# Kernel tuning notes

Measured on AMD Instinct MI355X. Metric: run time of the kernel, lower is better.

The kernel has to match this reference:

```python
import jax, jax.numpy as jnp
import numpy as np

B, T, C, H = 8, 2048, 1024, 64  # batch, block_size(=seq), embedding_dim, head_size

def setup_inputs() -> dict:
    key = jax.random.key(0)
    kx, kk, kq, kv = jax.random.split(key, 4)
    s = 1.0 / np.sqrt(C)
    return {
        "x": jax.random.normal(kx, (B, T, C), dtype=jnp.float32),
        "Wk": jax.random.normal(kk, (C, H), dtype=jnp.float32) * s,
        "Wq": jax.random.normal(kq, (C, H), dtype=jnp.float32) * s,
        "Wv": jax.random.normal(kv, (C, H), dtype=jnp.float32) * s,
    }

def reference(x, Wk, Wq, Wv):
    # projections: [B,T,C] @ [C,H] -> [B,T,H]
    k = jnp.einsum("btc,ch->bth", x, Wk)
    q = jnp.einsum("btc,ch->bth", x, Wq)
    v = jnp.einsum("btc,ch->bth", x, Wv)
    # scores: [B,T,T], scaled by head_size^-0.5
    wei = jnp.einsum("bth,bsh->bts", q, k) * (k.shape[-1] ** -0.5)
    # causal mask (lower-triangular keep)
    causal = jnp.tril(jnp.ones((T, T), dtype=bool))
    wei = jnp.where(causal[None, :, :], wei, -jnp.inf)
    wei = jax.nn.softmax(wei, axis=-1)
    # dropout_rate=0.0 -> identity
    out = jnp.einsum("bts,bsh->bth", wei, v)
    return out
```

## Files before the change

### kernel.cpp

```cpp
#include <hip/hip_runtime.h>

#define NB 8
#define NT 2048
#define NC 1024
#define NH 64
#define BT (NB*NT)

typedef __bf16 bf16x8 __attribute__((ext_vector_type(8)));
typedef float  f32x4  __attribute__((ext_vector_type(4)));
typedef unsigned short us8 __attribute__((ext_vector_type(8)));

__device__ __forceinline__ unsigned short f2bf(float f) {
  unsigned u = __builtin_bit_cast(unsigned, f);
  u = (u + 0x7FFFu + ((u >> 16) & 1u)) >> 16;
  return (unsigned short)u;
}

__device__ __forceinline__ bf16x8 ld_frag(const unsigned short* p) {
  return __builtin_bit_cast(bf16x8, *(const us8*)p);
}

__global__ __launch_bounds__(256) void wconv_kernel(
    const float* __restrict__ Wk, const float* __restrict__ Wq,
    const float* __restrict__ Wv, unsigned short* __restrict__ Wt)
{
  __shared__ unsigned short T[64][72];
  const int t = threadIdx.x;
  const int mat = blockIdx.x >> 4;
  const int k0 = (blockIdx.x & 15) * 64;
  const float* __restrict__ W = (mat == 0) ? Wq : (mat == 1) ? Wk : Wv;
  const int kk = t >> 2, h0 = (t & 3) * 16;
  const float* src = &W[(size_t)(k0 + kk) * NH + h0];
#pragma unroll
  for (int j = 0; j < 4; ++j) {
    const float4 v = *(const float4*)(src + j*4);
    T[h0 + j*4 + 0][kk] = f2bf(v.x);
    T[h0 + j*4 + 1][kk] = f2bf(v.y);
    T[h0 + j*4 + 2][kk] = f2bf(v.z);
    T[h0 + j*4 + 3][kk] = f2bf(v.w);
  }
  __syncthreads();
  const int h = t >> 2, c0 = (t & 3) * 16;
  unsigned short* dst = &Wt[(size_t)(mat*64 + h) * NC + k0 + c0];
  *(us8*)dst       = *(const us8*)&T[h][c0];
  *(us8*)(dst + 8) = *(const us8*)&T[h][c0 + 8];
}

__global__ __launch_bounds__(512) void proj_kernel(
    const float* __restrict__ x, const unsigned short* __restrict__ Wt,
    unsigned short* __restrict__ qkv)
{
  __shared__ unsigned short Asm[64][72];
  __shared__ unsigned short Bsm[192][72];

  const int t = threadIdx.x, w = t >> 6, lane = t & 63;
  const int wm = w >> 1, wn = w & 1;
  const int m0 = blockIdx.x * 64;
  const int fr = lane & 15, fo = (lane >> 4) * 8;

  f32x4 acc[6];
#pragma unroll
  for (int n = 0; n < 6; ++n) acc[n] = (f32x4){0.f, 0.f, 0.f, 0.f};

  const int ar = t >> 3, akc = (t & 7) * 8;

  for (int k0 = 0; k0 < NC; k0 += 64) {
    {
      const float* src = &x[(size_t)(m0 + ar) * NC + k0 + akc];
      const float4 a = *(const float4*)src;
      const float4 b = *(const float4*)(src + 4);
      us8 u;
      u[0]=f2bf(a.x); u[1]=f2bf(a.y); u[2]=f2bf(a.z); u[3]=f2bf(a.w);
      u[4]=f2bf(b.x); u[5]=f2bf(b.y); u[6]=f2bf(b.z); u[7]=f2bf(b.w);
      *(us8*)&Asm[ar][akc] = u;
    }
#pragma unroll
    for (int i = 0; i < 3; ++i) {
      const int c = t + 512*i, r = c >> 3, kc = (c & 7) * 8;
      *(us8*)&Bsm[r][kc] = *(const us8*)&Wt[(size_t)r * NC + k0 + kc];
    }
    __syncthreads();

    bf16x8 af[2], bfr[2][6];
#pragma unroll
    for (int ks = 0; ks < 2; ++ks) {
      af[ks] = ld_frag(&Asm[wm*16 + fr][ks*32 + fo]);
#pragma unroll
      for (int n = 0; n < 6; ++n) bfr[ks][n] = ld_frag(&Bsm[wn*96 + n*16 + fr][ks*32 + fo]);
    }
#pragma unroll
    for (int ks = 0; ks < 2; ++ks)
#pragma unroll
      for (int n = 0; n < 6; ++n)
        acc[n] = __builtin_amdgcn_mfma_f32_16x16x32_bf16(af[ks], bfr[ks][n], acc[n], 0, 0, 0);
    __syncthreads();
  }

  const int rg = (lane >> 4) * 4;
  const int trow = m0 + wm*16 + rg;
#pragma unroll
  for (int n = 0; n < 6; ++n) {
    const int col = wn*96 + n*16;
    const int mat = col >> 6;
    const int h = (col & 63) + fr;
    if (mat < 2) {
      unsigned short* op = qkv + (size_t)mat * BT * NH;
#pragma unroll
      for (int r = 0; r < 4; ++r)
        op[(size_t)(trow + r) * NH + h] = f2bf(acc[n][r]);
    } else {
      unsigned short* vt = qkv + (size_t)2 * BT * NH;
#pragma unroll
      for (int r = 0; r < 4; ++r)
        vt[(size_t)h * BT + trow + r] = f2bf(acc[n][r]);
    }
  }
}

__global__ __launch_bounds__(256) void attn_kernel(
    const unsigned short* __restrict__ qkv, float* __restrict__ out)
{
  __shared__ unsigned short Psm[4][16][72];
  __shared__ float co[4][16][68];
  __shared__ float cl[4][16];

  const int t = threadIdx.x, w = t >> 6, lane = t & 63;
  const int b = blockIdx.y;
  const unsigned short* __restrict__ qp = qkv;
  const unsigned short* __restrict__ kp = qkv + (size_t)BT * NH;
  const unsigned short* __restrict__ vt = qkv + (size_t)2 * BT * NH;
  const int fr = lane & 15, fo = (lane >> 4) * 8, rg = (lane >> 4) * 4;

#pragma unroll 1
  for (int ph = 0; ph < 2; ++ph) {
    const int j = ph ? (127 - (int)blockIdx.x) : (int)blockIdx.x;
    const int q0 = j * 16;
    const int ntiles = (j >> 2) + 1;

    bf16x8 aq0, aq1;
    {
      const size_t qoff = ((size_t)b * NT + q0 + fr) * NH;
      aq0 = ld_frag(&qp[qoff + fo]);
      aq1 = ld_frag(&qp[qoff + 32 + fo]);
    }

    f32x4 o[4];
#pragma unroll
    for (int n = 0; n < 4; ++n) o[n] = (f32x4){0.f, 0.f, 0.f, 0.f};
    float lp[4] = {0.f, 0.f, 0.f, 0.f};

    for (int kt = w; kt < ntiles; kt += 4) {
      const int kv0 = kt * 64;

      f32x4 s[4];
#pragma unroll
      for (int n = 0; n < 4; ++n) s[n] = (f32x4){0.f, 0.f, 0.f, 0.f};
#pragma unroll
      for (int n = 0; n < 4; ++n) {
        const size_t koff = ((size_t)b*NT + kv0 + n*16 + fr) * NH + fo;
        s[n] = __builtin_amdgcn_mfma_f32_16x16x32_bf16(aq0, ld_frag(&kp[koff]), s[n], 0, 0, 0);
        s[n] = __builtin_amdgcn_mfma_f32_16x16x32_bf16(aq1, ld_frag(&kp[koff + 32]), s[n], 0, 0, 0);
      }

#pragma unroll
      for (int n = 0; n < 4; ++n)
#pragma unroll
        for (int r = 0; r < 4; ++r) s[n][r] = __expf(s[n][r] * 0.125f);

      if (kt == ntiles - 1) {
#pragma unroll
        for (int n = 0; n < 4; ++n) {
          const int col = kv0 + n*16 + fr;
#pragma unroll
          for (int r = 0; r < 4; ++r)
            if (col > q0 + rg + r) s[n][r] = 0.f;
        }
      }

#pragma unroll
      for (int r = 0; r < 4; ++r)
        lp[r] += (s[0][r] + s[1][r]) + (s[2][r] + s[3][r]);

#pragma unroll
      for (int n = 0; n < 4; ++n)
#pragma unroll
        for (int r = 0; r < 4; ++r)
          Psm[w][rg + r][n*16 + fr] = f2bf(s[n][r]);

      bf16x8 pa0 = ld_frag(&Psm[w][fr][fo]);
      bf16x8 pa1 = ld_frag(&Psm[w][fr][32 + fo]);

#pragma unroll
      for (int n = 0; n < 4; ++n) {
        const size_t voff = (size_t)(n*16 + fr) * BT + (size_t)b*NT + kv0 + fo;
        o[n] = __builtin_amdgcn_mfma_f32_16x16x32_bf16(pa0, ld_frag(&vt[voff]), o[n], 0, 0, 0);
        o[n] = __builtin_amdgcn_mfma_f32_16x16x32_bf16(pa1, ld_frag(&vt[voff + 32]), o[n], 0, 0, 0);
      }
    }

#pragma unroll
    for (int r = 0; r < 4; ++r) {
#pragma unroll
      for (int off = 1; off < 16; off <<= 1) lp[r] += __shfl_xor(lp[r], off);
    }
    if (fr == 0) {
#pragma unroll
      for (int r = 0; r < 4; ++r) cl[w][rg + r] = lp[r];
    }
#pragma unroll
    for (int n = 0; n < 4; ++n)
#pragma unroll
      for (int r = 0; r < 4; ++r) co[w][rg + r][n*16 + fr] = o[n][r];
    __syncthreads();

    {
      const int row = t >> 4, c0 = (t & 15) * 4;
      const float l = (cl[0][row] + cl[1][row]) + (cl[2][row] + cl[3][row]);
      const float inv = 1.f / l;
      float4 ov;
      ov.x = ((co[0][row][c0+0] + co[1][row][c0+0]) + (co[2][row][c0+0] + co[3][row][c0+0])) * inv;
      ov.y = ((co[0][row][c0+1] + co[1][row][c0+1]) + (co[2][row][c0+1] + co[3][row][c0+1])) * inv;
      ov.z = ((co[0][row][c0+2] + co[1][row][c0+2]) + (co[2][row][c0+2] + co[3][row][c0+2])) * inv;
      ov.w = ((co[0][row][c0+3] + co[1][row][c0+3]) + (co[2][row][c0+3] + co[3][row][c0+3])) * inv;
      *(float4*)&out[((size_t)b*NT + q0 + row) * NH + c0] = ov;
    }
    if (ph == 0) __syncthreads();
  }
}

extern "C" void kernel_launch(void* const* d_in, const int* in_sizes, int n_in,
                              void* d_out, int out_size, void* d_ws, size_t ws_size,
                              hipStream_t stream) {
  (void)in_sizes; (void)n_in; (void)out_size; (void)ws_size;
  const float* x  = (const float*)d_in[0];
  const float* Wk = (const float*)d_in[1];
  const float* Wq = (const float*)d_in[2];
  const float* Wv = (const float*)d_in[3];
  unsigned short* qkv = (unsigned short*)d_ws;
  unsigned short* Wt  = qkv + (size_t)3 * BT * NH;

  wconv_kernel<<<48, 256, 0, stream>>>(Wk, Wq, Wv, Wt);
  proj_kernel<<<BT/64, 512, 0, stream>>>(x, Wt, qkv);
  attn_kernel<<<dim3(64, NB), 256, 0, stream>>>(qkv, (float*)d_out);
}
```

Before: 156.2 us.

## Drop LDS staging in projection, load fragments directly, remap attention blocks by batch

The projection kernel no longer stages x and W tiles through shared memory with block-wide barriers. Each wave now loads its bf16 fragments straight from global memory, with x converted to bf16 in registers, in 256-thread blocks. V output is transposed through a small per-wave LDS buffer so it can be written with vector stores instead of scattered 2-byte stores. The attention grid is relinearized so adjacent blocks cover different batches, which balances work across CUs. The trade is redundant global/L2 reads of W and x fragments in place of shared reuse.

```diff
diff --git a/kernel.cpp b/kernel.cpp
--- a/kernel.cpp
+++ b/kernel.cpp
@@ -46,74 +46,70 @@
   *(us8*)(dst + 8) = *(const us8*)&T[h][c0 + 8];
 }
 
-__global__ __launch_bounds__(512) void proj_kernel(
+__global__ __launch_bounds__(256) void proj_kernel(
     const float* __restrict__ x, const unsigned short* __restrict__ Wt,
     unsigned short* __restrict__ qkv)
 {
-  __shared__ unsigned short Asm[64][72];
-  __shared__ unsigned short Bsm[192][72];
+  __shared__ unsigned short Vb[4][64][18];
 
   const int t = threadIdx.x, w = t >> 6, lane = t & 63;
-  const int wm = w >> 1, wn = w & 1;
-  const int m0 = blockIdx.x * 64;
-  const int fr = lane & 15, fo = (lane >> 4) * 8;
+  const int W = blockIdx.x * 4 + w;
+  const int row0 = (W >> 1) * 16;
+  const int cb = (W & 1) * 96;
+  const int fr = lane & 15, fo = (lane >> 4) * 8, rg = (lane >> 4) * 4;
 
   f32x4 acc[6];
 #pragma unroll
   for (int n = 0; n < 6; ++n) acc[n] = (f32x4){0.f, 0.f, 0.f, 0.f};
 
-  const int ar = t >> 3, akc = (t & 7) * 8;
+  const float* __restrict__ xrow = &x[(size_t)(row0 + fr) * NC];
 
   for (int k0 = 0; k0 < NC; k0 += 64) {
-    {
-      const float* src = &x[(size_t)(m0 + ar) * NC + k0 + akc];
-      const float4 a = *(const float4*)src;
-      const float4 b = *(const float4*)(src + 4);
-      us8 u;
-      u[0]=f2bf(a.x); u[1]=f2bf(a.y); u[2]=f2bf(a.z); u[3]=f2bf(a.w);
-      u[4]=f2bf(b.x); u[5]=f2bf(b.y); u[6]=f2bf(b.z); u[7]=f2bf(b.w);
-      *(us8*)&Asm[ar][akc] = u;
-    }
-#pragma unroll
-    for (int i = 0; i < 3; ++i) {
-      const int c = t + 512*i, r = c >> 3, kc = (c & 7) * 8;
-      *(us8*)&Bsm[r][kc] = *(const us8*)&Wt[(size_t)r * NC + k0 + kc];
-    }
-    __syncthreads();
-
-    bf16x8 af[2], bfr[2][6];
+    bf16x8 af[2];
 #pragma unroll
     for (int ks = 0; ks < 2; ++ks) {
-      af[ks] = ld_frag(&Asm[wm*16 + fr][ks*32 + fo]);
-#pragma unroll
-      for (int n = 0; n < 6; ++n) bfr[ks][n] = ld_frag(&Bsm[wn*96 + n*16 + fr][ks*32 + fo]);
-    }
+      const float* p = xrow + k0 + ks*32 + fo;
+      const float4 a = *(const float4*)p;
+      const float4 b = *(const float4*)(p + 4);
+      bf16x8 v;
+      v[0] = (__bf16)a.x; v[1] = (__bf16)a.y; v[2] = (__bf16)a.z; v[3] = (__bf16)a.w;
+      v[4] = (__bf16)b.x; v[5] = (__bf16)b.y; v[6] = (__bf16)b.z; v[7] = (__bf16)b.w;
+      af[ks] = v;
+    }
+    bf16x8 bfr[2][6];
+#pragma unroll
+    for (int ks = 0; ks < 2; ++ks)
+#pragma unroll
+      for (int n = 0; n < 6; ++n)
+        bfr[ks][n] = ld_frag(&Wt[(size_t)(cb + n*16 + fr) * NC + k0 + ks*32 + fo]);
 #pragma unroll
     for (int ks = 0; ks < 2; ++ks)
 #pragma unroll
       for (int n = 0; n < 6; ++n)
         acc[n] = __builtin_amdgcn_mfma_f32_16x16x32_bf16(af[ks], bfr[ks][n], acc[n], 0, 0, 0);
-    __syncthreads();
-  }
-
-  const int rg = (lane >> 4) * 4;
-  const int trow = m0 + wm*16 + rg;
+  }
+
 #pragma unroll
   for (int n = 0; n < 6; ++n) {
-    const int col = wn*96 + n*16;
-    const int mat = col >> 6;
-    const int h = (col & 63) + fr;
-    if (mat < 2) {
+    const int col = cb + n*16;
+    if (col < 128) {
+      const int mat = col >> 6;
       unsigned short* op = qkv + (size_t)mat * BT * NH;
+      const int h = (col & 63) + fr;
 #pragma unroll
       for (int r = 0; r < 4; ++r)
-        op[(size_t)(trow + r) * NH + h] = f2bf(acc[n][r]);
+        op[(size_t)(row0 + rg + r) * NH + h] = f2bf(acc[n][r]);
     } else {
-      unsigned short* vt = qkv + (size_t)2 * BT * NH;
 #pragma unroll
       for (int r = 0; r < 4; ++r)
-        vt[(size_t)h * BT + trow + r] = f2bf(acc[n][r]);
-    }
+        Vb[w][(col - 128) + fr][rg + r] = f2bf(acc[n][r]);
+    }
+  }
+  if (cb == 96) {
+    unsigned short* vt = qkv + (size_t)2 * BT * NH;
+    unsigned short* dst = &vt[(size_t)lane * BT + row0];
+    *(us8*)dst       = *(const us8*)&Vb[w][lane][0];
+    *(us8*)(dst + 8) = *(const us8*)&Vb[w][lane][8];
   }
 }
 
@@ -125,7 +121,9 @@
   __shared__ float cl[4][16];
 
   const int t = threadIdx.x, w = t >> 6, lane = t & 63;
-  const int b = blockIdx.y;
+  const int lin = blockIdx.x + 64 * blockIdx.y;
+  const int b = lin & 7;
+  const int j0 = lin >> 3;
   const unsigned short* __restrict__ qp = qkv;
   const unsigned short* __restrict__ kp = qkv + (size_t)BT * NH;
   const unsigned short* __restrict__ vt = qkv + (size_t)2 * BT * NH;
@@ -133,7 +131,7 @@
 
 #pragma unroll 1
   for (int ph = 0; ph < 2; ++ph) {
-    const int j = ph ? (127 - (int)blockIdx.x) : (int)blockIdx.x;
+    const int j = ph ? (127 - j0) : j0;
     const int q0 = j * 16;
     const int ntiles = (j >> 2) + 1;
 
@@ -240,6 +238,6 @@
   unsigned short* Wt  = qkv + (size_t)3 * BT * NH;
 
   wconv_kernel<<<48, 256, 0, stream>>>(Wk, Wq, Wv, Wt);
-  proj_kernel<<<BT/64, 512, 0, stream>>>(x, Wt, qkv);
+  proj_kernel<<<BT/32, 256, 0, stream>>>(x, Wt, qkv);
   attn_kernel<<<dim3(64, NB), 256, 0, stream>>>(qkv, (float*)d_out);
 }
```

After: 184.6 us. 1.18x slower.
